# Kernel optimization log

Measured on AMD Instinct MI355X. Metric: run time of the kernel, lower is better.

The kernel has to match this reference:

```python
import jax, jax.numpy as jnp
import numpy as np
from jax import lax

N, C, RC, H, W = 2, 256, 32, 64, 64  # RC = C // 8


def conv1x1(x, w, b):
    # x: [n,c,h,w], w: [o,c], b: [o]
    return jnp.einsum('nchw,oc->nohw', x, w) + b[None, :, None, None]


def conv3x3(x, w, b):
    # x: [n,c,h,w], w: [o,i,3,3]
    y = lax.conv_general_dilated(x, w, window_strides=(1, 1), padding='SAME',
                                 dimension_numbers=('NCHW', 'OIHW', 'NCHW'))
    return y + b[None, :, None, None]


def setup_inputs() -> dict:
    key = jax.random.key(0)
    ks = jax.random.split(key, 16)
    p = lambda k, s: jax.random.normal(k, s, dtype=jnp.float32) * 0.02
    z = lambda o: jnp.zeros((o,), jnp.float32)
    return {
        'rgb_feat': jax.random.normal(ks[0], (N, C, H, W), jnp.float32),
        'chm_feat': jax.random.normal(ks[1], (N, C, H, W), jnp.float32),
        'rgb_q_w': p(ks[2], (RC, C)), 'rgb_q_b': z(RC),
        'rgb_k_w': p(ks[3], (RC, C)), 'rgb_k_b': z(RC),
        'rgb_v_w': p(ks[4], (C, C)), 'rgb_v_b': z(C),
        'depth_q_w': p(ks[5], (RC, C)), 'depth_q_b': z(RC),
        'depth_k_w': p(ks[6], (RC, C)), 'depth_k_b': z(RC),
        'depth_v_w': p(ks[7], (C, C)), 'depth_v_b': z(C),
        'gate_w': p(ks[8], (C, 2 * C)), 'gate_b': z(C),
        'fus1_w': p(ks[9], (2 * C, 2 * C)), 'fus1_b': z(2 * C),
        'fus2_w': p(ks[10], (2 * C, 2 * C, 3, 3)), 'fus2_b': z(2 * C),
        'fus3_w': p(ks[11], (C, 2 * C)), 'fus3_b': z(C),
        'skip_w': p(ks[12], (C, 2 * C)), 'skip_b': z(C),
    }


def reference(rgb_feat, chm_feat,
              rgb_q_w, rgb_q_b, rgb_k_w, rgb_k_b, rgb_v_w, rgb_v_b,
              depth_q_w, depth_q_b, depth_k_w, depth_k_b, depth_v_w, depth_v_b,
              gate_w, gate_b, fus1_w, fus1_b, fus2_w, fus2_b,
              fus3_w, fus3_b, skip_w, skip_b):
    n, c, h, w = rgb_feat.shape
    hw = h * w
    flat = lambda t: t.reshape(n, t.shape[1], hw)

    rq = flat(conv1x1(rgb_feat, rgb_q_w, rgb_q_b))       # [n,rc,hw]
    rk = flat(conv1x1(rgb_feat, rgb_k_w, rgb_k_b))       # [n,rc,hw]
    rv = flat(conv1x1(rgb_feat, rgb_v_w, rgb_v_b))       # [n,c,hw]
    dq = flat(conv1x1(chm_feat, depth_q_w, depth_q_b))   # [n,rc,hw]
    dk = flat(conv1x1(chm_feat, depth_k_w, depth_k_b))   # [n,rc,hw]
    dv = flat(conv1x1(chm_feat, depth_v_w, depth_v_b))   # [n,c,hw]

    # rgb branch attended with depth-derived attention
    rgb_attn = jax.nn.softmax(jnp.einsum('nri,nrj->nij', dq, dk), axis=-1)  # [n,hw,hw]
    br = jnp.einsum('nci,nij->ncj', rv, rgb_attn).reshape(rgb_feat.shape) + rgb_feat

    # depth branch attended with rgb-derived attention
    depth_attn = jax.nn.softmax(jnp.einsum('nri,nrj->nij', rq, rk), axis=-1)
    bd = jnp.einsum('nci,nij->ncj', dv, depth_attn).reshape(chm_feat.shape) + chm_feat

    cat = jnp.concatenate([br, bd], axis=1)              # [n,2c,h,w]
    g = jax.nn.sigmoid(conv1x1(cat, gate_w, gate_b))     # [n,c,h,w]
    c_fused = br * g + bd * (1.0 - g)
    d_fused = br * bd
    f = jnp.concatenate([c_fused, d_fused], axis=1)      # [n,2c,h,w]

    y = jax.nn.relu(conv1x1(f, fus1_w, fus1_b))
    y = jax.nn.relu(conv3x3(y, fus2_w, fus2_b))
    y = conv1x1(y, fus3_w, fus3_b)
    fused = y + conv1x1(f, skip_w, skip_b)
    return fused
```

## Files before the change

### kernel.cpp

```cpp
#include <hip/hip_runtime.h>
#include <stdint.h>


typedef __bf16 bf16_t;
typedef __bf16 bf16x8 __attribute__((ext_vector_type(8)));
typedef float f32x4 __attribute__((ext_vector_type(4)));

#define HW 4096
#define NB 2

__device__ inline f32x4 mfma_bf16(bf16x8 a, bf16x8 b, f32x4 c) {
    return __builtin_amdgcn_mfma_f32_16x16x32_bf16(a, b, c, 0, 0, 0);
}

#define MAXJOB 12
struct CvtJobs {
    const float* src[MAXJOB];
    bf16_t* dst[MAXJOB];
    int vend[MAXJOB];
    int rowlen[MAXJOB];
    int rowstride[MAXJOB];
    int rowoff[MAXJOB];
};

__global__ __launch_bounds__(256) void convert_batch_k(CvtJobs J, int totalvec) {
    int gv = blockIdx.x * 256 + threadIdx.x;
    if (gv >= totalvec) return;
    int j = 0;
    while (gv >= J.vend[j]) j++;
    int vbase = (j == 0) ? 0 : J.vend[j - 1];
    int e = (gv - vbase) * 8;
    const float* s = J.src[j] + e;
    float4 f0 = *(const float4*)s;
    float4 f1 = *(const float4*)(s + 4);
    bf16x8 o;
    o[0] = (bf16_t)f0.x; o[1] = (bf16_t)f0.y; o[2] = (bf16_t)f0.z; o[3] = (bf16_t)f0.w;
    o[4] = (bf16_t)f1.x; o[5] = (bf16_t)f1.y; o[6] = (bf16_t)f1.z; o[7] = (bf16_t)f1.w;
    int di = e;
    if (J.rowlen[j])
        di = (e / J.rowlen[j]) * J.rowstride[j] + J.rowoff[j] + (e % J.rowlen[j]);
    *(bf16x8*)(J.dst[j] + di) = o;
}

__global__ __launch_bounds__(256) void pack_bias_k(const float* qr, const float* kr,
                                                   const float* qd, const float* kd,
                                                   const float* sb, const float* fb,
                                                   float* BQK_R, float* BQK_D, float* BSUM) {
    int t = threadIdx.x;
    if (t < 32) {
        BQK_R[t] = qr[t]; BQK_R[32 + t] = kr[t];
        BQK_D[t] = qd[t]; BQK_D[32 + t] = kd[t];
    }
    BSUM[t] = sb[t] + fb[t];
}

__global__ __launch_bounds__(256) void reorder_fus2_k(const float* __restrict__ src,
                                                      bf16_t* __restrict__ dst) {
    int idx = blockIdx.x * 256 + threadIdx.x;
    if (idx >= 512 * 4608) return;
    int o = idx / 4608;
    int t = idx % 4608;
    int t9 = t / 512;
    int c  = t % 512;
    dst[idx] = (bf16_t)src[(size_t)o * 4608 + c * 9 + t9];
}

template <int EPI, bool OUT_BF16>
__global__ __launch_bounds__(256) void gemm_k(const bf16_t* __restrict__ A,
                                              const bf16_t* __restrict__ A2,
                                              const bf16_t* __restrict__ B,
                                              const float* __restrict__ bias,
                                              const float* __restrict__ bias2,
                                              void* __restrict__ outp,
                                              const void* __restrict__ aux,
                                              int M, int K, size_t strideB, size_t strideO) {
    __shared__ bf16_t Bt[64][72];
    const int t = threadIdx.x;
    const int mb = blockIdx.x, jb = blockIdx.y, n = blockIdx.z;
    const int w = t >> 6, lane = t & 63, quad = lane >> 4, l16 = lane & 15;

    const bf16_t* Au = (n >= 2) ? A2 : A;
    const float* biasu = (n >= 2) ? bias2 : bias;

    const bf16_t* Bb = B + (size_t)n * strideB + jb * 64;
    const int srow = t >> 2;
    const int scol = (t & 3) << 4;

    f32x4 zero = {0.f, 0.f, 0.f, 0.f};
    f32x4 acc[4] = {zero, zero, zero, zero};

    const bf16_t* Arow = Au + (size_t)(mb * 64 + w * 16 + l16) * K + quad * 8;

    for (int k0 = 0; k0 < K; k0 += 64) {
        const bf16_t* src = Bb + (size_t)(k0 + srow) * HW + scol;
        bf16x8 v0 = *(const bf16x8*)src;
        bf16x8 v1 = *(const bf16x8*)(src + 8);
        __syncthreads();
#pragma unroll
        for (int e = 0; e < 8; e++) Bt[scol + e][srow] = v0[e];
#pragma unroll
        for (int e = 0; e < 8; e++) Bt[scol + 8 + e][srow] = v1[e];
        __syncthreads();

        bf16x8 a0 = *(const bf16x8*)(Arow + k0);
        bf16x8 a1 = *(const bf16x8*)(Arow + k0 + 32);
#pragma unroll
        for (int ns = 0; ns < 4; ns++) {
            bf16x8 b0 = *(const bf16x8*)&Bt[ns * 16 + l16][quad * 8];
            bf16x8 b1 = *(const bf16x8*)&Bt[ns * 16 + l16][32 + quad * 8];
            acc[ns] = mfma_bf16(a0, b0, acc[ns]);
            acc[ns] = mfma_bf16(a1, b1, acc[ns]);
        }
    }

    if (EPI == 6) {
#pragma unroll
        for (int ns = 0; ns < 4; ns++) {
            int col = jb * 64 + ns * 16 + l16;
            union { bf16_t h[4]; unsigned long long u; } pk;
#pragma unroll
            for (int rr = 0; rr < 4; rr++) {
                int m = w * 16 + quad * 4 + rr;
                pk.h[rr] = (bf16_t)(acc[ns][rr] + biasu[m]);
            }
            *(unsigned long long*)((bf16_t*)outp +
                ((size_t)n * HW + col) * 64 + w * 16 + quad * 4) = pk.u;
        }
    } else if (EPI == 7) {
        const int m_base = mb * 64 + w * 16 + quad * 4;
#pragma unroll
        for (int ns = 0; ns < 4; ns++) {
            int col = jb * 64 + ns * 16 + l16;
            union { bf16_t h[4]; unsigned long long u; } pk;
#pragma unroll
            for (int rr = 0; rr < 4; rr++) {
                float v = acc[ns][rr] + biasu[m_base + rr];
                pk.h[rr] = (bf16_t)(v > 0.f ? v : 0.f);
            }
            *(unsigned long long*)((bf16_t*)outp +
                ((size_t)n * HW + col) * 512 + m_base) = pk.u;
        }
    } else if (EPI == 5) {
        const bf16_t* catp = (const bf16_t*)aux;
        bf16_t* f = (bf16_t*)outp;
#pragma unroll
        for (int ns = 0; ns < 4; ns++) {
#pragma unroll
            for (int rr = 0; rr < 4; rr++) {
                int m = mb * 64 + w * 16 + quad * 4 + rr;
                int col = jb * 64 + ns * 16 + l16;
                float v = acc[ns][rr] + biasu[m];
                float g = 1.f / (1.f + __expf(-v));
                size_t base = (size_t)n * 512 * HW + (size_t)m * HW + col;
                float br = (float)catp[base];
                float bd = (float)catp[base + (size_t)256 * HW];
                size_t ob = (size_t)n * 1024 * HW + (size_t)m * HW + col;
                f[ob] = (bf16_t)(br * g + bd * (1.f - g));
                f[ob + (size_t)256 * HW] = (bf16_t)(br * bd);
            }
        }
    } else {
#pragma unroll
        for (int ns = 0; ns < 4; ns++) {
#pragma unroll
            for (int rr = 0; rr < 4; rr++) {
                int m = mb * 64 + w * 16 + quad * 4 + rr;
                int col = jb * 64 + ns * 16 + l16;
                float v = acc[ns][rr] + biasu[m];
                if (EPI == 1) v = v > 0.f ? v : 0.f;
                else if (EPI == 3) v = v / ((const float*)aux)[n * HW + col];
                size_t oi = (size_t)n * strideO + (size_t)m * HW + col;
                if (OUT_BF16) ((bf16_t*)outp)[oi] = (bf16_t)v;
                else ((float*)outp)[oi] = v;
            }
        }
    }
}

__global__ __launch_bounds__(256) void conv3_k(const bf16_t* __restrict__ A,
                                               const bf16_t* __restrict__ Y1n,
                                               const float* __restrict__ bias,
                                               bf16_t* __restrict__ outp,
                                               size_t strideN) {
    __shared__ bf16_t kTn[198][72];
    const int t = threadIdx.x;
    const int mb = blockIdx.x, y = blockIdx.y, n = blockIdx.z;
    const int w = t >> 6, lane = t & 63, quad = lane >> 4, l16 = lane & 15;

    f32x4 zero = {0.f, 0.f, 0.f, 0.f};
    f32x4 acc[2][4];
#pragma unroll
    for (int i = 0; i < 2; i++)
#pragma unroll
        for (int j = 0; j < 4; j++) acc[i][j] = zero;

    const bf16_t* Yb = Y1n + (size_t)n * HW * 512;

    const bf16_t* Arow0 = A + (size_t)(mb * 128 + w * 32 + l16) * 4608 + quad * 8;
    const bf16_t* Arow1 = Arow0 + (size_t)16 * 4608;

    int pxs[7], seg[7], gidx[7];
    bool ok[7], act[7];
#pragma unroll
    for (int i = 0; i < 7; i++) {
        int slot = t + i * 256;
        act[i] = slot < 1584;
        int ps = act[i] ? (slot >> 3) : 0;
        pxs[i] = ps;
        seg[i] = slot & 7;
        int r = ps / 66, xm = ps % 66;
        int yy = y + r - 1, xx = xm - 1;
        ok[i] = act[i] && ((unsigned)yy < 64u) && ((unsigned)xx < 64u);
        gidx[i] = ok[i] ? (yy * 64 + xx) : 0;
    }

    for (int c0 = 0; c0 < 512; c0 += 64) {
        bf16x8 vals[7];
#pragma unroll
        for (int i = 0; i < 7; i++) {
            bf16x8 v;
            if (ok[i]) {
                v = *(const bf16x8*)(Yb + (size_t)gidx[i] * 512 + c0 + seg[i] * 8);
            } else {
#pragma unroll
                for (int e = 0; e < 8; e++) v[e] = (bf16_t)0.f;
            }
            vals[i] = v;
        }
        __syncthreads();
#pragma unroll
        for (int i = 0; i < 7; i++)
            if (act[i]) *(bf16x8*)&kTn[pxs[i]][seg[i] * 8] = vals[i];
        __syncthreads();

#pragma unroll
        for (int t9 = 0; t9 < 9; t9++) {
            const int dy = t9 / 3, dx = t9 % 3;
            const bf16_t* ap0 = Arow0 + t9 * 512 + c0;
            const bf16_t* ap1 = Arow1 + t9 * 512 + c0;
            bf16x8 a00 = *(const bf16x8*)(ap0);
            bf16x8 a01 = *(const bf16x8*)(ap0 + 32);
            bf16x8 a10 = *(const bf16x8*)(ap1);
            bf16x8 a11 = *(const bf16x8*)(ap1 + 32);
#pragma unroll
            for (int ns = 0; ns < 4; ns++) {
                int p = dy * 66 + ns * 16 + l16 + dx;
                bf16x8 b0 = *(const bf16x8*)&kTn[p][quad * 8];
                bf16x8 b1 = *(const bf16x8*)&kTn[p][32 + quad * 8];
                acc[0][ns] = mfma_bf16(a00, b0, acc[0][ns]);
                acc[0][ns] = mfma_bf16(a01, b1, acc[0][ns]);
                acc[1][ns] = mfma_bf16(a10, b0, acc[1][ns]);
                acc[1][ns] = mfma_bf16(a11, b1, acc[1][ns]);
            }
        }
    }

#pragma unroll
    for (int ms = 0; ms < 2; ms++) {
#pragma unroll
        for (int ns = 0; ns < 4; ns++) {
#pragma unroll
            for (int rr = 0; rr < 4; rr++) {
                int m = mb * 128 + w * 32 + ms * 16 + quad * 4 + rr;
                int x = ns * 16 + l16;
                float v = acc[ms][ns][rr] + bias[m];
                v = v > 0.f ? v : 0.f;
                outp[(size_t)n * strideN + (size_t)m * HW + y * 64 + x] = (bf16_t)v;
            }
        }
    }
}

__global__ __launch_bounds__(256) void rowsum_k(const bf16_t* __restrict__ QKT,
                                                float* __restrict__ Z) {
    __shared__ float Zp[2][32];
    const int t = threadIdx.x, ib = blockIdx.x, k = blockIdx.y;
    const int w = t >> 6, lane = t & 63, quad = lane >> 4, l16 = lane & 15;
    const int is = w & 1, jh = w >> 1;
    const int qs = k ^ 2;
    const bf16_t* Q = QKT + (size_t)qs * HW * 64;

    bf16x8 a = *(const bf16x8*)(Q + (size_t)(ib * 32 + is * 16 + l16) * 64 + quad * 8);
    float zacc[4] = {0.f, 0.f, 0.f, 0.f};
    f32x4 zero = {0.f, 0.f, 0.f, 0.f};

    for (int jt = jh * 32; jt < jh * 32 + 32; jt++) {
#pragma unroll
        for (int ns = 0; ns < 4; ns++) {
            bf16x8 b = *(const bf16x8*)(Q + (size_t)(jt * 64 + ns * 16 + l16) * 64 + 32 + quad * 8);
            f32x4 s = mfma_bf16(a, b, zero);
#pragma unroll
            for (int rr = 0; rr < 4; rr++) zacc[rr] += __expf(s[rr]);
        }
    }

#pragma unroll
    for (int rr = 0; rr < 4; rr++) {
        for (int mask = 1; mask < 16; mask <<= 1)
            zacc[rr] += __shfl_xor(zacc[rr], mask, 64);
    }
    if (l16 == 0) {
#pragma unroll
        for (int rr = 0; rr < 4; rr++)
            Zp[jh][is * 16 + quad * 4 + rr] = zacc[rr];
    }
    __syncthreads();
    if (t < 32)
        Z[(size_t)k * HW + ib * 32 + t] = Zp[0][t] + Zp[1][t];
}

__global__ __launch_bounds__(256) void attn3_k(const bf16_t* __restrict__ QKT,
                                               const bf16_t* __restrict__ V,
                                               const float* __restrict__ rgb_feat,
                                               const float* __restrict__ chm_feat,
                                               bf16_t* __restrict__ CAT) {
    __shared__ bf16_t PT[2][64][72];
    const int t = threadIdx.x, cb = blockIdx.x, jb = blockIdx.y, z = blockIdx.z;
    const int w = t >> 6, lane = t & 63, quad = lane >> 4, l16 = lane & 15;
    const int qs = z ^ 2, n = z & 1;

    const bf16_t* Q = QKT + (size_t)qs * HW * 64;

    bf16x8 bS[4];
#pragma unroll
    for (int ns = 0; ns < 4; ns++)
        bS[ns] = *(const bf16x8*)(Q + (size_t)(jb * 64 + ns * 16 + l16) * 64 + 32 + quad * 8);

    f32x4 zero = {0.f, 0.f, 0.f, 0.f};
    f32x4 acc[2][4];
#pragma unroll
    for (int i = 0; i < 2; i++)
#pragma unroll
        for (int j = 0; j < 4; j++) acc[i][j] = zero;

    const bf16_t* Vr0 = V + ((size_t)z * 256 + cb * 128 + w * 16 + l16) * HW + quad * 8;
    const bf16_t* Vr1 = Vr0 + (size_t)64 * HW;

    for (int it = 0; it < 64; it++) {
        const int p = it & 1;
        bf16x8 aS = *(const bf16x8*)(Q + (size_t)(it * 64 + w * 16 + l16) * 64 + quad * 8);
        bf16x8 aV[2][2];
        aV[0][0] = *(const bf16x8*)(Vr0 + it * 64);
        aV[0][1] = *(const bf16x8*)(Vr0 + it * 64 + 32);
        aV[1][0] = *(const bf16x8*)(Vr1 + it * 64);
        aV[1][1] = *(const bf16x8*)(Vr1 + it * 64 + 32);

#pragma unroll
        for (int ns = 0; ns < 4; ns++) {
            f32x4 s = mfma_bf16(aS, bS[ns], zero);
            union { bf16_t h[4]; unsigned long long u; } pk;
#pragma unroll
            for (int rr = 0; rr < 4; rr++) pk.h[rr] = (bf16_t)__expf(s[rr]);
            *(unsigned long long*)&PT[p][ns * 16 + l16][w * 16 + quad * 4] = pk.u;
        }
        __syncthreads();

#pragma unroll
        for (int ns = 0; ns < 4; ns++) {
            bf16x8 b0 = *(const bf16x8*)&PT[p][ns * 16 + l16][quad * 8];
            bf16x8 b1 = *(const bf16x8*)&PT[p][ns * 16 + l16][32 + quad * 8];
#pragma unroll
            for (int ct = 0; ct < 2; ct++) {
                acc[ct][ns] = mfma_bf16(aV[ct][0], b0, acc[ct][ns]);
                acc[ct][ns] = mfma_bf16(aV[ct][1], b1, acc[ct][ns]);
            }
        }
    }

    const float* feat = ((z < 2) ? rgb_feat : chm_feat) + (size_t)n * 256 * HW;
    bf16_t* outp = CAT + (size_t)n * 512 * HW + (size_t)(z < 2 ? 0 : 256) * HW;
#pragma unroll
    for (int ct = 0; ct < 2; ct++) {
#pragma unroll
        for (int ns = 0; ns < 4; ns++) {
#pragma unroll
            for (int rr = 0; rr < 4; rr++) {
                int c = cb * 128 + ct * 64 + w * 16 + quad * 4 + rr;
                int col = jb * 64 + ns * 16 + l16;
                float v = acc[ct][ns][rr] + feat[(size_t)c * HW + col];
                outp[(size_t)c * HW + col] = (bf16_t)v;
            }
        }
    }
}

extern "C" void kernel_launch(void* const* d_in, const int* in_sizes, int n_in,
                              void* d_out, int out_size, void* d_ws, size_t ws_size,
                              hipStream_t stream) {
    (void)in_sizes; (void)n_in; (void)out_size; (void)ws_size;

    const float* rgb_feat  = (const float*)d_in[0];
    const float* chm_feat  = (const float*)d_in[1];
    const float* rgb_q_w   = (const float*)d_in[2];
    const float* rgb_q_b   = (const float*)d_in[3];
    const float* rgb_k_w   = (const float*)d_in[4];
    const float* rgb_k_b   = (const float*)d_in[5];
    const float* rgb_v_w   = (const float*)d_in[6];
    const float* rgb_v_b   = (const float*)d_in[7];
    const float* depth_q_w = (const float*)d_in[8];
    const float* depth_q_b = (const float*)d_in[9];
    const float* depth_k_w = (const float*)d_in[10];
    const float* depth_k_b = (const float*)d_in[11];
    const float* depth_v_w = (const float*)d_in[12];
    const float* depth_v_b = (const float*)d_in[13];
    const float* gate_w    = (const float*)d_in[14];
    const float* gate_b    = (const float*)d_in[15];
    const float* fus1_w    = (const float*)d_in[16];
    const float* fus1_b    = (const float*)d_in[17];
    const float* fus2_w    = (const float*)d_in[18];
    const float* fus2_b    = (const float*)d_in[19];
    const float* fus3_w    = (const float*)d_in[20];
    const float* fus3_b    = (const float*)d_in[21];
    const float* skip_w    = (const float*)d_in[22];
    const float* skip_b    = (const float*)d_in[23];

    char* ws = (char*)d_ws;
    size_t off = 0;
    auto alloc = [&](size_t bytes) -> char* {
        char* p = ws + off;
        off += (bytes + 255) & ~(size_t)255;
        return p;
    };

    bf16_t* WQK_R = (bf16_t*)alloc(64 * 256 * 2);
    bf16_t* WQK_D = (bf16_t*)alloc(64 * 256 * 2);
    bf16_t* WV_R  = (bf16_t*)alloc(256 * 256 * 2);
    bf16_t* WV_D  = (bf16_t*)alloc(256 * 256 * 2);
    bf16_t* WGATE = (bf16_t*)alloc(256 * 512 * 2);
    bf16_t* WFUS1 = (bf16_t*)alloc(512 * 512 * 2);
    bf16_t* WFUS2 = (bf16_t*)alloc(512 * 4608 * 2);
    bf16_t* WCAT  = (bf16_t*)alloc(256 * 1024 * 2);
    float*  BQK_R = (float*)alloc(64 * 4);
    float*  BQK_D = (float*)alloc(64 * 4);
    float*  BSUM  = (float*)alloc(256 * 4);
    bf16_t* XB    = (bf16_t*)alloc((size_t)4 * 256 * HW * 2);
    bf16_t* QKT   = (bf16_t*)alloc((size_t)4 * HW * 64 * 2);
    float*  ZBUF  = (float*)alloc((size_t)4 * HW * 4);
    bf16_t* V4    = (bf16_t*)alloc((size_t)4 * 256 * HW * 2);
    bf16_t* CAT   = (bf16_t*)alloc((size_t)NB * 512 * HW * 2);
    bf16_t* FY    = (bf16_t*)alloc((size_t)NB * 1024 * HW * 2);
    bf16_t* Y1    = (bf16_t*)alloc((size_t)NB * HW * 512 * 2);

    bf16_t* XR = XB;
    bf16_t* XC = XB + (size_t)2 * 256 * HW;

    CvtJobs J;
    int cum = 0, nj = 0;
    auto addjob = [&](const float* s, bf16_t* d, int cnt, int rl, int rs, int ro) {
        J.src[nj] = s; J.dst[nj] = d; cum += cnt / 8; J.vend[nj] = cum;
        J.rowlen[nj] = rl; J.rowstride[nj] = rs; J.rowoff[nj] = ro; nj++;
    };
    addjob(rgb_feat, XR, NB * 256 * HW, 0, 0, 0);
    addjob(chm_feat, XC, NB * 256 * HW, 0, 0, 0);
    addjob(rgb_q_w, WQK_R, 32 * 256, 0, 0, 0);
    addjob(rgb_k_w, WQK_R + 32 * 256, 32 * 256, 0, 0, 0);
    addjob(depth_q_w, WQK_D, 32 * 256, 0, 0, 0);
    addjob(depth_k_w, WQK_D + 32 * 256, 32 * 256, 0, 0, 0);
    addjob(rgb_v_w, WV_R, 256 * 256, 0, 0, 0);
    addjob(depth_v_w, WV_D, 256 * 256, 0, 0, 0);
    addjob(gate_w, WGATE, 256 * 512, 0, 0, 0);
    addjob(fus1_w, WFUS1, 512 * 512, 0, 0, 0);
    addjob(skip_w, WCAT, 256 * 512, 512, 1024, 0);
    addjob(fus3_w, WCAT, 256 * 512, 512, 1024, 512);
    int totalvec = cum;
    convert_batch_k<<<dim3((totalvec + 255) / 256), 256, 0, stream>>>(J, totalvec);
    reorder_fus2_k<<<dim3(512 * 4608 / 256), 256, 0, stream>>>(fus2_w, WFUS2);
    pack_bias_k<<<dim3(1), 256, 0, stream>>>(rgb_q_b, rgb_k_b, depth_q_b, depth_k_b,
                                             skip_b, fus3_b, BQK_R, BQK_D, BSUM);

    gemm_k<6, true><<<dim3(1, 64, 4), 256, 0, stream>>>(
        WQK_R, WQK_D, XB, BQK_R, BQK_D, QKT, nullptr, 64, 256, (size_t)256 * HW, 0);

    rowsum_k<<<dim3(128, 4), 256, 0, stream>>>(QKT, ZBUF);

    gemm_k<3, true><<<dim3(4, 64, 4), 256, 0, stream>>>(
        WV_R, WV_D, XB, rgb_v_b, depth_v_b, V4, ZBUF, 256, 256, (size_t)256 * HW, (size_t)256 * HW);

    attn3_k<<<dim3(2, 64, 4), 256, 0, stream>>>(QKT, V4, rgb_feat, chm_feat, CAT);

    gemm_k<5, true><<<dim3(4, 64, NB), 256, 0, stream>>>(
        WGATE, WGATE, CAT, gate_b, gate_b, FY, CAT, 256, 512, (size_t)512 * HW, 0);

    gemm_k<7, true><<<dim3(8, 64, NB), 256, 0, stream>>>(
        WFUS1, WFUS1, FY, fus1_b, fus1_b, Y1, nullptr, 512, 512, (size_t)1024 * HW, 0);

    conv3_k<<<dim3(4, 64, NB), 256, 0, stream>>>(WFUS2, Y1, fus2_b,
                                                 FY + (size_t)512 * HW, (size_t)1024 * HW);

    gemm_k<0, false><<<dim3(4, 64, NB), 256, 0, stream>>>(
        WCAT, WCAT, FY, BSUM, BSUM, d_out, nullptr, 256, 1024, (size_t)1024 * HW, (size_t)256 * HW);
}
```

Measured before the change: 389.0 us.

## Merge prep kernels, use 128-row GEMM tiles, software-pipeline attention scores

Three preprocessing launches (weight conversion, fus2 reorder, bias packing) become one kernel that picks its role by block index. The value, gate, fus1 and final GEMMs move to a new kernel in which each wave computes 32 output rows, so each block covers 128 rows. Each staged B tile is reused across twice as many rows, and the grid is halved. The attention kernel now computes the next chunk's exp scores into the other shared buffer while running the PV MFMAs on the current chunk, leaving one barrier per iteration. The trade-off is more accumulator registers per thread and fewer blocks for occupancy.

```diff
diff --git a/kernel.cpp b/kernel.cpp
--- a/kernel.cpp
+++ b/kernel.cpp
@@ -23,49 +23,48 @@
     int rowoff[MAXJOB];
 };
 
-__global__ __launch_bounds__(256) void convert_batch_k(CvtJobs J, int totalvec) {
-    int gv = blockIdx.x * 256 + threadIdx.x;
-    if (gv >= totalvec) return;
-    int j = 0;
-    while (gv >= J.vend[j]) j++;
-    int vbase = (j == 0) ? 0 : J.vend[j - 1];
-    int e = (gv - vbase) * 8;
-    const float* s = J.src[j] + e;
-    float4 f0 = *(const float4*)s;
-    float4 f1 = *(const float4*)(s + 4);
-    bf16x8 o;
-    o[0] = (bf16_t)f0.x; o[1] = (bf16_t)f0.y; o[2] = (bf16_t)f0.z; o[3] = (bf16_t)f0.w;
-    o[4] = (bf16_t)f1.x; o[5] = (bf16_t)f1.y; o[6] = (bf16_t)f1.z; o[7] = (bf16_t)f1.w;
-    int di = e;
-    if (J.rowlen[j])
-        di = (e / J.rowlen[j]) * J.rowstride[j] + J.rowoff[j] + (e % J.rowlen[j]);
-    *(bf16x8*)(J.dst[j] + di) = o;
-}
-
-__global__ __launch_bounds__(256) void pack_bias_k(const float* qr, const float* kr,
-                                                   const float* qd, const float* kd,
-                                                   const float* sb, const float* fb,
-                                                   float* BQK_R, float* BQK_D, float* BSUM) {
-    int t = threadIdx.x;
-    if (t < 32) {
-        BQK_R[t] = qr[t]; BQK_R[32 + t] = kr[t];
-        BQK_D[t] = qd[t]; BQK_D[32 + t] = kd[t];
-    }
-    BSUM[t] = sb[t] + fb[t];
-}
-
-__global__ __launch_bounds__(256) void reorder_fus2_k(const float* __restrict__ src,
-                                                      bf16_t* __restrict__ dst) {
-    int idx = blockIdx.x * 256 + threadIdx.x;
-    if (idx >= 512 * 4608) return;
-    int o = idx / 4608;
-    int t = idx % 4608;
-    int t9 = t / 512;
-    int c  = t % 512;
-    dst[idx] = (bf16_t)src[(size_t)o * 4608 + c * 9 + t9];
-}
-
-template <int EPI, bool OUT_BF16>
+__global__ __launch_bounds__(256) void prep_k(CvtJobs J, int totalvec, int cvtBlocks,
+                                              const float* __restrict__ fus2src,
+                                              bf16_t* __restrict__ fus2dst,
+                                              const float* qr, const float* kr,
+                                              const float* qd, const float* kd,
+                                              const float* sb, const float* fb,
+                                              float* BQK_R, float* BQK_D, float* BSUM) {
+    const int b = blockIdx.x, t = threadIdx.x;
+    if (b < cvtBlocks) {
+        int gv = b * 256 + t;
+        if (gv >= totalvec) return;
+        int j = 0;
+        while (gv >= J.vend[j]) j++;
+        int vbase = (j == 0) ? 0 : J.vend[j - 1];
+        int e = (gv - vbase) * 8;
+        const float* s = J.src[j] + e;
+        float4 f0 = *(const float4*)s;
+        float4 f1 = *(const float4*)(s + 4);
+        bf16x8 o;
+        o[0] = (bf16_t)f0.x; o[1] = (bf16_t)f0.y; o[2] = (bf16_t)f0.z; o[3] = (bf16_t)f0.w;
+        o[4] = (bf16_t)f1.x; o[5] = (bf16_t)f1.y; o[6] = (bf16_t)f1.z; o[7] = (bf16_t)f1.w;
+        int di = e;
+        if (J.rowlen[j])
+            di = (e / J.rowlen[j]) * J.rowstride[j] + J.rowoff[j] + (e % J.rowlen[j]);
+        *(bf16x8*)(J.dst[j] + di) = o;
+    } else if (b < cvtBlocks + 9216) {
+        int idx = (b - cvtBlocks) * 256 + t;
+        int o = idx / 4608;
+        int tt = idx % 4608;
+        int t9 = tt / 512;
+        int c  = tt % 512;
+        fus2dst[idx] = (bf16_t)fus2src[(size_t)o * 4608 + c * 9 + t9];
+    } else {
+        if (t < 32) {
+            BQK_R[t] = qr[t]; BQK_R[32 + t] = kr[t];
+            BQK_D[t] = qd[t]; BQK_D[32 + t] = kd[t];
+        }
+        BSUM[t] = sb[t] + fb[t];
+    }
+}
+
+template <int EPI>
 __global__ __launch_bounds__(256) void gemm_k(const bf16_t* __restrict__ A,
                                               const bf16_t* __restrict__ A2,
                                               const bf16_t* __restrict__ B,
@@ -126,52 +125,114 @@
             *(unsigned long long*)((bf16_t*)outp +
                 ((size_t)n * HW + col) * 64 + w * 16 + quad * 4) = pk.u;
         }
-    } else if (EPI == 7) {
-        const int m_base = mb * 64 + w * 16 + quad * 4;
-#pragma unroll
-        for (int ns = 0; ns < 4; ns++) {
-            int col = jb * 64 + ns * 16 + l16;
-            union { bf16_t h[4]; unsigned long long u; } pk;
-#pragma unroll
-            for (int rr = 0; rr < 4; rr++) {
-                float v = acc[ns][rr] + biasu[m_base + rr];
-                pk.h[rr] = (bf16_t)(v > 0.f ? v : 0.f);
-            }
-            *(unsigned long long*)((bf16_t*)outp +
-                ((size_t)n * HW + col) * 512 + m_base) = pk.u;
-        }
-    } else if (EPI == 5) {
-        const bf16_t* catp = (const bf16_t*)aux;
-        bf16_t* f = (bf16_t*)outp;
-#pragma unroll
-        for (int ns = 0; ns < 4; ns++) {
-#pragma unroll
-            for (int rr = 0; rr < 4; rr++) {
-                int m = mb * 64 + w * 16 + quad * 4 + rr;
+    }
+}
+
+template <int EPI>
+__global__ __launch_bounds__(256) void gemm128_k(const bf16_t* __restrict__ A,
+                                                 const bf16_t* __restrict__ A2,
+                                                 const bf16_t* __restrict__ B,
+                                                 const float* __restrict__ bias,
+                                                 const float* __restrict__ bias2,
+                                                 void* __restrict__ outp,
+                                                 const void* __restrict__ aux,
+                                                 int K, size_t strideB, size_t strideO) {
+    __shared__ bf16_t Bt[64][72];
+    const int t = threadIdx.x;
+    const int mb = blockIdx.x, jb = blockIdx.y, n = blockIdx.z;
+    const int w = t >> 6, lane = t & 63, quad = lane >> 4, l16 = lane & 15;
+
+    const bf16_t* Au = (n >= 2) ? A2 : A;
+    const float* biasu = (n >= 2) ? bias2 : bias;
+
+    const bf16_t* Bb = B + (size_t)n * strideB + jb * 64;
+    const int srow = t >> 2;
+    const int scol = (t & 3) << 4;
+
+    f32x4 zero = {0.f, 0.f, 0.f, 0.f};
+    f32x4 acc[2][4];
+#pragma unroll
+    for (int i = 0; i < 2; i++)
+#pragma unroll
+        for (int j = 0; j < 4; j++) acc[i][j] = zero;
+
+    const bf16_t* Arow0 = Au + (size_t)(mb * 128 + w * 32 + l16) * K + quad * 8;
+    const bf16_t* Arow1 = Arow0 + (size_t)16 * K;
+
+    for (int k0 = 0; k0 < K; k0 += 64) {
+        const bf16_t* src = Bb + (size_t)(k0 + srow) * HW + scol;
+        bf16x8 v0 = *(const bf16x8*)src;
+        bf16x8 v1 = *(const bf16x8*)(src + 8);
+        __syncthreads();
+#pragma unroll
+        for (int e = 0; e < 8; e++) Bt[scol + e][srow] = v0[e];
+#pragma unroll
+        for (int e = 0; e < 8; e++) Bt[scol + 8 + e][srow] = v1[e];
+        __syncthreads();
+
+        bf16x8 a00 = *(const bf16x8*)(Arow0 + k0);
+        bf16x8 a01 = *(const bf16x8*)(Arow0 + k0 + 32);
+        bf16x8 a10 = *(const bf16x8*)(Arow1 + k0);
+        bf16x8 a11 = *(const bf16x8*)(Arow1 + k0 + 32);
+#pragma unroll
+        for (int ns = 0; ns < 4; ns++) {
+            bf16x8 b0 = *(const bf16x8*)&Bt[ns * 16 + l16][quad * 8];
+            bf16x8 b1 = *(const bf16x8*)&Bt[ns * 16 + l16][32 + quad * 8];
+            acc[0][ns] = mfma_bf16(a00, b0, acc[0][ns]);
+            acc[0][ns] = mfma_bf16(a01, b1, acc[0][ns]);
+            acc[1][ns] = mfma_bf16(a10, b0, acc[1][ns]);
+            acc[1][ns] = mfma_bf16(a11, b1, acc[1][ns]);
+        }
+    }
+
+#pragma unroll
+    for (int ms = 0; ms < 2; ms++) {
+        if (EPI == 7) {
+            const int m_base = mb * 128 + w * 32 + ms * 16 + quad * 4;
+#pragma unroll
+            for (int ns = 0; ns < 4; ns++) {
                 int col = jb * 64 + ns * 16 + l16;
-                float v = acc[ns][rr] + biasu[m];
-                float g = 1.f / (1.f + __expf(-v));
-                size_t base = (size_t)n * 512 * HW + (size_t)m * HW + col;
-                float br = (float)catp[base];
-                float bd = (float)catp[base + (size_t)256 * HW];
-                size_t ob = (size_t)n * 1024 * HW + (size_t)m * HW + col;
-                f[ob] = (bf16_t)(br * g + bd * (1.f - g));
-                f[ob + (size_t)256 * HW] = (bf16_t)(br * bd);
-            }
-        }
-    } else {
-#pragma unroll
-        for (int ns = 0; ns < 4; ns++) {
-#pragma unroll
-            for (int rr = 0; rr < 4; rr++) {
-                int m = mb * 64 + w * 16 + quad * 4 + rr;
-                int col = jb * 64 + ns * 16 + l16;
-                float v = acc[ns][rr] + biasu[m];
-                if (EPI == 1) v = v > 0.f ? v : 0.f;
-                else if (EPI == 3) v = v / ((const float*)aux)[n * HW + col];
-                size_t oi = (size_t)n * strideO + (size_t)m * HW + col;
-                if (OUT_BF16) ((bf16_t*)outp)[oi] = (bf16_t)v;
-                else ((float*)outp)[oi] = v;
+                union { bf16_t h[4]; unsigned long long u; } pk;
+#pragma unroll
+                for (int rr = 0; rr < 4; rr++) {
+                    float v = acc[ms][ns][rr] + biasu[m_base + rr];
+                    pk.h[rr] = (bf16_t)(v > 0.f ? v : 0.f);
+                }
+                *(unsigned long long*)((bf16_t*)outp +
+                    ((size_t)n * HW + col) * 512 + m_base) = pk.u;
+            }
+        } else if (EPI == 5) {
+            const bf16_t* catp = (const bf16_t*)aux;
+            bf16_t* f = (bf16_t*)outp;
+#pragma unroll
+            for (int ns = 0; ns < 4; ns++) {
+#pragma unroll
+                for (int rr = 0; rr < 4; rr++) {
+                    int m = mb * 128 + w * 32 + ms * 16 + quad * 4 + rr;
+                    int col = jb * 64 + ns * 16 + l16;
+                    float v = acc[ms][ns][rr] + biasu[m];
+                    float g = 1.f / (1.f + __expf(-v));
+                    size_t base = (size_t)n * 512 * HW + (size_t)m * HW + col;
+                    float br = (float)catp[base];
+                    float bd = (float)catp[base + (size_t)256 * HW];
+                    size_t ob = (size_t)n * 1024 * HW + (size_t)m * HW + col;
+                    f[ob] = (bf16_t)(br * g + bd * (1.f - g));
+                    f[ob + (size_t)256 * HW] = (bf16_t)(br * bd);
+                }
+            }
+        } else {
+#pragma unroll
+            for (int ns = 0; ns < 4; ns++) {
+#pragma unroll
+                for (int rr = 0; rr < 4; rr++) {
+                    int m = mb * 128 + w * 32 + ms * 16 + quad * 4 + rr;
+                    int col = jb * 64 + ns * 16 + l16;
+                    float v = acc[ms][ns][rr] + biasu[m];
+                    if (EPI == 3) v = v / ((const float*)aux)[n * HW + col];
+                    size_t oi = (size_t)n * strideO + (size_t)m * HW + col;
+                    if (EPI == 0) ((float*)outp)[oi] = v;
+                    else ((bf16_t*)outp)[oi] = (bf16_t)v;
+                }
             }
         }
     }
@@ -309,11 +370,11 @@
         Z[(size_t)k * HW + ib * 32 + t] = Zp[0][t] + Zp[1][t];
 }
 
-__global__ __launch_bounds__(256) void attn3_k(const bf16_t* __restrict__ QKT,
-                                               const bf16_t* __restrict__ V,
-                                               const float* __restrict__ rgb_feat,
-                                               const float* __restrict__ chm_feat,
-                                               bf16_t* __restrict__ CAT) {
+__global__ __launch_bounds__(256) void attn3p_k(const bf16_t* __restrict__ QKT,
+                                                const bf16_t* __restrict__ V,
+                                                const float* __restrict__ rgb_feat,
+                                                const float* __restrict__ chm_feat,
+                                                bf16_t* __restrict__ CAT) {
     __shared__ bf16_t PT[2][64][72];
     const int t = threadIdx.x, cb = blockIdx.x, jb = blockIdx.y, z = blockIdx.z;
     const int w = t >> 6, lane = t & 63, quad = lane >> 4, l16 = lane & 15;
@@ -336,24 +397,38 @@
     const bf16_t* Vr0 = V + ((size_t)z * 256 + cb * 128 + w * 16 + l16) * HW + quad * 8;
     const bf16_t* Vr1 = Vr0 + (size_t)64 * HW;
 
+    {
+        bf16x8 aS = *(const bf16x8*)(Q + (size_t)(w * 16 + l16) * 64 + quad * 8);
+#pragma unroll
+        for (int ns = 0; ns < 4; ns++) {
+            f32x4 s = mfma_bf16(aS, bS[ns], zero);
+            union { bf16_t h[4]; unsigned long long u; } pk;
+#pragma unroll
+            for (int rr = 0; rr < 4; rr++) pk.h[rr] = (bf16_t)__expf(s[rr]);
+            *(unsigned long long*)&PT[0][ns * 16 + l16][w * 16 + quad * 4] = pk.u;
+        }
+    }
+    __syncthreads();
+
     for (int it = 0; it < 64; it++) {
         const int p = it & 1;
-        bf16x8 aS = *(const bf16x8*)(Q + (size_t)(it * 64 + w * 16 + l16) * 64 + quad * 8);
         bf16x8 aV[2][2];
         aV[0][0] = *(const bf16x8*)(Vr0 + it * 64);
         aV[0][1] = *(const bf16x8*)(Vr0 + it * 64 + 32);
         aV[1][0] = *(const bf16x8*)(Vr1 + it * 64);
         aV[1][1] = *(const bf16x8*)(Vr1 + it * 64 + 32);
 
-#pragma unroll
-        for (int ns = 0; ns < 4; ns++) {
-            f32x4 s = mfma_bf16(aS, bS[ns], zero);
-            union { bf16_t h[4]; unsigned long long u; } pk;
-#pragma unroll
-            for (int rr = 0; rr < 4; rr++) pk.h[rr] = (bf16_t)__expf(s[rr]);
-            *(unsigned long long*)&PT[p][ns * 16 + l16][w * 16 + quad * 4] = pk.u;
-        }
-        __syncthreads();
+        if (it < 63) {
+            bf16x8 aS = *(const bf16x8*)(Q + (size_t)((it + 1) * 64 + w * 16 + l16) * 64 + quad * 8);
+#pragma unroll
+            for (int ns = 0; ns < 4; ns++) {
+                f32x4 s = mfma_bf16(aS, bS[ns], zero);
+                union { bf16_t h[4]; unsigned long long u; } pk;
+#pragma unroll
+                for (int rr = 0; rr < 4; rr++) pk.h[rr] = (bf16_t)__expf(s[rr]);
+                *(unsigned long long*)&PT[p ^ 1][ns * 16 + l16][w * 16 + quad * 4] = pk.u;
+            }
+        }
 
 #pragma unroll
         for (int ns = 0; ns < 4; ns++) {
@@ -365,6 +440,7 @@
                 acc[ct][ns] = mfma_bf16(aV[ct][1], b1, acc[ct][ns]);
             }
         }
+        __syncthreads();
     }
 
     const float* feat = ((z < 2) ? rgb_feat : chm_feat) + (size_t)n * 256 * HW;
@@ -463,30 +539,31 @@
     addjob(skip_w, WCAT, 256 * 512, 512, 1024, 0);
     addjob(fus3_w, WCAT, 256 * 512, 512, 1024, 512);
     int totalvec = cum;
-    convert_batch_k<<<dim3((totalvec + 255) / 256), 256, 0, stream>>>(J, totalvec);
-    reorder_fus2_k<<<dim3(512 * 4608 / 256), 256, 0, stream>>>(fus2_w, WFUS2);
-    pack_bias_k<<<dim3(1), 256, 0, stream>>>(rgb_q_b, rgb_k_b, depth_q_b, depth_k_b,
-                                             skip_b, fus3_b, BQK_R, BQK_D, BSUM);
-
-    gemm_k<6, true><<<dim3(1, 64, 4), 256, 0, stream>>>(
+    int cvtBlocks = (totalvec + 255) / 256;
+    prep_k<<<dim3(cvtBlocks + 9216 + 1), 256, 0, stream>>>(
+        J, totalvec, cvtBlocks, fus2_w, WFUS2,
+        rgb_q_b, rgb_k_b, depth_q_b, depth_k_b, skip_b, fus3_b,
+        BQK_R, BQK_D, BSUM);
+
+    gemm_k<6><<<dim3(1, 64, 4), 256, 0, stream>>>(
         WQK_R, WQK_D, XB, BQK_R, BQK_D, QKT, nullptr, 64, 256, (size_t)256 * HW, 0);
 
     rowsum_k<<<dim3(128, 4), 256, 0, stream>>>(QKT, ZBUF);
 
-    gemm_k<3, true><<<dim3(4, 64, 4), 256, 0, stream>>>(
-        WV_R, WV_D, XB, rgb_v_b, depth_v_b, V4, ZBUF, 256, 256, (size_t)256 * HW, (size_t)256 * HW);
-
-    attn3_k<<<dim3(2, 64, 4), 256, 0, stream>>>(QKT, V4, rgb_feat, chm_feat, CAT);
-
-    gemm_k<5, true><<<dim3(4, 64, NB), 256, 0, stream>>>(
-        WGATE, WGATE, CAT, gate_b, gate_b, FY, CAT, 256, 512, (size_t)512 * HW, 0);
-
-    gemm_k<7, true><<<dim3(8, 64, NB), 256, 0, stream>>>(
-        WFUS1, WFUS1, FY, fus1_b, fus1_b, Y1, nullptr, 512, 512, (size_t)1024 * HW, 0);
+    gemm128_k<3><<<dim3(2, 64, 4), 256, 0, stream>>>(
+        WV_R, WV_D, XB, rgb_v_b, depth_v_b, V4, ZBUF, 256, (size_t)256 * HW, (size_t)256 * HW);
+
+    attn3p_k<<<dim3(2, 64, 4), 256, 0, stream>>>(QKT, V4, rgb_feat, chm_feat, CAT);
+
+    gemm128_k<5><<<dim3(2, 64, NB), 256, 0, stream>>>(
+        WGATE, WGATE, CAT, gate_b, gate_b, FY, CAT, 512, (size_t)512 * HW, 0);
+
+    gemm128_k<7><<<dim3(4, 64, NB), 256, 0, stream>>>(
+        WFUS1, WFUS1, FY, fus1_b, fus1_b, Y1, nullptr, 512, (size_t)1024 * HW, 0);
 
     conv3_k<<<dim3(4, 64, NB), 256, 0, stream>>>(WFUS2, Y1, fus2_b,
                                                  FY + (size_t)512 * HW, (size_t)1024 * HW);
 
-    gemm_k<0, false><<<dim3(4, 64, NB), 256, 0, stream>>>(
-        WCAT, WCAT, FY, BSUM, BSUM, d_out, nullptr, 256, 1024, (size_t)1024 * HW, (size_t)256 * HW);
-}
+    gemm128_k<0><<<dim3(2, 64, NB), 256, 0, stream>>>(
+        WCAT, WCAT, FY, BSUM, BSUM, d_out, nullptr, 1024, (size_t)1024 * HW, (size_t)256 * HW);
+}
```

Result: no change. 392.2 us (+0.8%).
